# Kernel optimization log

Hardware: AMD Instinct MI355X
Metric: run time of the kernel (lower is better)

Reference implementation:

```python
import jax, jax.numpy as jnp
import numpy as np

N, E, L, D_IN = 20000, 320000, 3, 128
K, H = 8, 64
NEG_SLOPE = 0.01


def setup_inputs() -> dict:
    key = jax.random.key(0)
    k1, k2, k3, k4, k5, k6 = jax.random.split(key, 6)
    return {
        "node_feat": jax.random.normal(k1, (N, D_IN), jnp.float32),
        "edge_feat": jax.random.normal(k2, (E, L, D_IN), jnp.float32),
        "W_enc": jax.random.normal(k3, (D_IN, K * H), jnp.float32) * (1.0 / np.sqrt(D_IN)),
        "attn_l": jax.random.normal(k4, (1, K, H), jnp.float32) * 0.1,
        "W_r": jax.random.normal(k5, (K, D_IN), jnp.float32) * (1.0 / np.sqrt(D_IN)),
        "dst": jax.random.randint(k6, (E,), 0, N, jnp.int32),
    }


def reference(node_feat, edge_feat, W_enc, attn_l, W_r, dst):
    n = node_feat.shape[0]
    e_cnt = edge_feat.shape[0]
    # metapath instance encoder ('linear'): mean over metapath length, then project
    ft = jnp.mean(edge_feat, axis=1) @ W_enc            # (E, K*H)
    ft = ft.reshape(e_cnt, K, H)                        # (E, K, H)
    # per-edge / per-dst attention logits
    el = jnp.sum(ft * attn_l, axis=-1)                  # (E, K)
    er = node_feat @ W_r.T                              # (N, K)
    e = jax.nn.leaky_relu(el + er[dst], negative_slope=NEG_SLOPE)  # (E, K)
    # edge_softmax: segmented (per destination node) stable softmax
    seg_max = jax.ops.segment_max(e, dst, num_segments=n)
    seg_max = jnp.where(jnp.isfinite(seg_max), seg_max, 0.0)
    ex = jnp.exp(e - seg_max[dst])                      # (E, K)
    seg_sum = jax.ops.segment_sum(ex, dst, num_segments=n)
    a = ex / seg_sum[dst]                               # (E, K)  (attn_drop=0 in eval)
    # weighted scatter-sum of edge features into destination nodes
    out = jax.ops.segment_sum(ft * a[..., None], dst, num_segments=n)  # (N, K, H)
    return out
```

## Files before the change

### kernel.cpp

```cpp
#include <hip/hip_runtime.h>
#include <math.h>

#define NN   20000
#define EE   320000
#define DIN  128
#define KK   8
#define HH   64
#define NEG  0.01f
#define CAP  128

typedef __attribute__((ext_vector_type(8))) short short8;
typedef __attribute__((ext_vector_type(4))) float f32x4;

__device__ __forceinline__ unsigned short f2bf(float f) {
  unsigned u = __float_as_uint(f);
  u += 0x7FFF + ((u >> 16) & 1);
  return (unsigned short)(u >> 16);
}
__device__ __forceinline__ float bf2f_lo(unsigned u) {
  return __uint_as_float(u << 16);
}
__device__ __forceinline__ float bf2f_hi(unsigned u) {
  return __uint_as_float(u & 0xFFFF0000u);
}

__device__ __forceinline__ float wave_sum(float v) {
#pragma unroll
  for (int m = 1; m < 64; m <<= 1) v += __shfl_xor(v, m, 64);
  return v;
}

__global__ __launch_bounds__(256) void k_pre(const float* __restrict__ W_enc,
                                             const float* __restrict__ attn_l,
                                             const float* __restrict__ node_feat,
                                             const float* __restrict__ W_r,
                                             unsigned short* __restrict__ Wt,
                                             unsigned short* __restrict__ Vt,
                                             float* __restrict__ er) {
  __shared__ __align__(16) float4 wr4[KK * 32];
  int b = blockIdx.x, tid = threadIdx.x;
  if (b < 256) {
    int gid = b * 256 + tid;
    int row = gid >> 7, d = gid & 127;
    Wt[gid] = f2bf(W_enc[(size_t)d * 512 + row]);
  } else if (b < 264) {
    int gid = (b - 256) * 256 + tid;
    int n = gid >> 7, d = gid & 127;
    float acc = 0.f;
    if (n < 8) {
#pragma unroll 8
      for (int h = 0; h < HH; ++h)
        acc += W_enc[(size_t)d * 512 + n * 64 + h] * attn_l[n * 64 + h];
    }
    Vt[gid] = f2bf(acc);
  } else {
    wr4[tid] = ((const float4*)W_r)[tid];
    __syncthreads();
    int gid = (b - 264) * 256 + tid;
    int n = gid >> 3, k = gid & 7;
    if (n < NN) {
      const float4* nf4 = (const float4*)node_feat + (size_t)n * 32;
      float acc = 0.f;
#pragma unroll
      for (int i = 0; i < 32; ++i) {
        float4 a = nf4[i], bb = wr4[k * 32 + i];
        acc += a.x * bb.x + a.y * bb.y + a.z * bb.z + a.w * bb.w;
      }
      er[gid] = acc;
    }
  }
}

__global__ __launch_bounds__(256) void k_mlog(const float* __restrict__ ef,
                                              const unsigned short* __restrict__ Vt,
                                              const float* __restrict__ er,
                                              const int* __restrict__ dst,
                                              unsigned short* __restrict__ x,
                                              float* __restrict__ e_log,
                                              int* __restrict__ counts) {
  __shared__ __align__(16) uint4 xl4[16 * 17];
  int tid = threadIdx.x;
  size_t gid = (size_t)blockIdx.x * 256 + tid;
  size_t e = gid >> 4;
  int s = gid & 15;
  const float4* p = (const float4*)(ef + e * 384) + s * 2;
  float4 a0 = p[0],  a1 = p[1];
  float4 b0 = p[32], b1 = p[33];
  float4 c0 = p[64], c1 = p[65];
  const float i3 = 1.f / 3.f;
  float m0 = (a0.x + b0.x + c0.x) * i3, m1 = (a0.y + b0.y + c0.y) * i3;
  float m2 = (a0.z + b0.z + c0.z) * i3, m3 = (a0.w + b0.w + c0.w) * i3;
  float m4 = (a1.x + b1.x + c1.x) * i3, m5 = (a1.y + b1.y + c1.y) * i3;
  float m6 = (a1.z + b1.z + c1.z) * i3, m7 = (a1.w + b1.w + c1.w) * i3;
  uint4 o;
  o.x = (unsigned)f2bf(m0) | ((unsigned)f2bf(m1) << 16);
  o.y = (unsigned)f2bf(m2) | ((unsigned)f2bf(m3) << 16);
  o.z = (unsigned)f2bf(m4) | ((unsigned)f2bf(m5) << 16);
  o.w = (unsigned)f2bf(m6) | ((unsigned)f2bf(m7) << 16);
  ((uint4*)x)[gid] = o;
  xl4[(tid >> 4) * 17 + (tid & 15)] = o;
  __syncthreads();

  if (tid < 64) {
    int lane = tid;
    int m = lane & 15, quad = lane >> 4;
    size_t e0 = (size_t)blockIdx.x * 16;
    const short8* xr = (const short8*)((const unsigned short*)xl4 + m * 136);
    const short8* vr = (const short8*)(Vt + (size_t)m * 128);
    f32x4 acc = {0.f, 0.f, 0.f, 0.f};
#pragma unroll
    for (int kt = 0; kt < 4; ++kt) {
      short8 a = xr[kt * 4 + quad];
      short8 bfr = vr[kt * 4 + quad];
      acc = __builtin_amdgcn_mfma_f32_16x16x32_bf16(a, bfr, acc, 0, 0, 0);
    }
    if (m < 8) {
#pragma unroll
      for (int r = 0; r < 4; ++r) {
        size_t ee = e0 + quad * 4 + r;
        int dv = dst[ee];
        float z = acc[r] + er[(size_t)dv * 8 + m];
        z = z > 0.f ? z : NEG * z;
        e_log[ee * 8 + m] = z;
        if (m == 0) atomicAdd(&counts[dv], 1);
      }
    }
  }
}

__device__ __forceinline__ int block_excl_scan256(int v, int tid) {
  __shared__ int wtot[4];
  int lane = tid & 63, wid = tid >> 6;
  int incl = v;
#pragma unroll
  for (int off = 1; off < 64; off <<= 1) {
    int t = __shfl_up(incl, off, 64);
    if (lane >= off) incl += t;
  }
  if (lane == 63) wtot[wid] = incl;
  __syncthreads();
  if (tid == 0) {
    int s = 0;
#pragma unroll
    for (int i = 0; i < 4; ++i) { int t = wtot[i]; wtot[i] = s; s += t; }
  }
  __syncthreads();
  return wtot[wid] + incl - v;
}

__global__ __launch_bounds__(256) void k_scan1(const int* __restrict__ counts,
                                               int* __restrict__ lexcl,
                                               int* __restrict__ btot) {
  int b = blockIdx.x, tid = threadIdx.x;
  int i = b * 256 + tid;
  int v = (i < NN) ? counts[i] : 0;
  int ex = block_excl_scan256(v, tid);
  lexcl[i] = ex;
  if (tid == 255) btot[b] = ex + v;
}

__global__ __launch_bounds__(256) void k_scan2(int* __restrict__ btot,
                                               int* __restrict__ bbase,
                                               int* __restrict__ offs) {
  int tid = threadIdx.x;
  int v = (tid < 80) ? btot[tid] : 0;
  int ex = block_excl_scan256(v, tid);
  if (tid < 80) bbase[tid] = ex;
  if (tid == 0) offs[NN] = EE;
}

__global__ __launch_bounds__(256) void k_scan3(const int* __restrict__ lexcl,
                                               const int* __restrict__ bbase,
                                               int* __restrict__ offs,
                                               int* __restrict__ cursor) {
  int b = blockIdx.x, tid = threadIdx.x;
  int i = b * 256 + tid;
  if (i < NN) {
    int o = lexcl[i] + bbase[b];
    offs[i] = o;
    cursor[i] = o;
  }
}

__global__ __launch_bounds__(256) void k_fill(const int* __restrict__ dst,
                                              int* __restrict__ cursor,
                                              int* __restrict__ elist) {
  int e = blockIdx.x * 256 + threadIdx.x;
  if (e < EE) {
    int p = atomicAdd(&cursor[dst[e]], 1);
    elist[p] = e;
  }
}

__global__ __launch_bounds__(256) void k_agg(const int* __restrict__ offs,
                                             const int* __restrict__ elist,
                                             const float* __restrict__ e_log,
                                             const unsigned short* __restrict__ x,
                                             unsigned short* __restrict__ y) {
  __shared__ float red[4][8];
  __shared__ float maxs[8], invs[8];
  __shared__ int eids[CAP];
  __shared__ __align__(16) float w[CAP * 8];
  __shared__ __align__(16) float xs[32 * 128];
  int n = blockIdx.x;
  int tid = threadIdx.x, lane = tid & 63, wid = tid >> 6;
  int start = offs[n], end = offs[n + 1];
  int cnt = end - start;
  int d = tid & 127, kg = tid >> 7;
  float acc0 = 0.f, acc1 = 0.f, acc2 = 0.f, acc3 = 0.f;

  if (cnt <= CAP) {
    for (int i = tid; i < cnt; i += 256) eids[i] = elist[start + i];
    __syncthreads();
    for (int j = tid; j < cnt * 2; j += 256)
      ((float4*)w)[j] = ((const float4*)e_log)[(size_t)eids[j >> 1] * 2 + (j & 1)];
    __syncthreads();

    int k = tid & 7, ib = tid >> 3;
    float mm = -3.4e38f;
    for (int i = ib; i < cnt; i += 32) mm = fmaxf(mm, w[i * 8 + k]);
    mm = fmaxf(mm, __shfl_xor(mm, 8, 64));
    mm = fmaxf(mm, __shfl_xor(mm, 16, 64));
    mm = fmaxf(mm, __shfl_xor(mm, 32, 64));
    if ((lane >> 3) == 0) red[wid][lane] = mm;
    __syncthreads();
    if (tid < 8)
      maxs[tid] = fmaxf(fmaxf(red[0][tid], red[1][tid]), fmaxf(red[2][tid], red[3][tid]));
    __syncthreads();

    float mk = maxs[k];
    float ss = 0.f;
    for (int i = ib; i < cnt; i += 32) {
      float v = __expf(w[i * 8 + k] - mk);
      w[i * 8 + k] = v;
      ss += v;
    }
    ss += __shfl_xor(ss, 8, 64);
    ss += __shfl_xor(ss, 16, 64);
    ss += __shfl_xor(ss, 32, 64);
    if ((lane >> 3) == 0) red[wid][lane] = ss;
    __syncthreads();
    if (tid < 8) {
      float tot = red[0][tid] + red[1][tid] + red[2][tid] + red[3][tid];
      invs[tid] = tot > 0.f ? 1.f / tot : 0.f;
    }
    __syncthreads();
    float iv = invs[k];
    for (int i = ib; i < cnt; i += 32) w[i * 8 + k] *= iv;
    __syncthreads();

    for (int base = 0; base < cnt; base += 32) {
      int nb = min(32, cnt - base);
      for (int j = tid; j < nb * 16; j += 256) {
        size_t e = (size_t)eids[base + (j >> 4)];
        uint4 t = ((const uint4*)x)[e * 16 + (j & 15)];
        float4 lo = make_float4(bf2f_lo(t.x), bf2f_hi(t.x), bf2f_lo(t.y), bf2f_hi(t.y));
        float4 hi = make_float4(bf2f_lo(t.z), bf2f_hi(t.z), bf2f_lo(t.w), bf2f_hi(t.w));
        ((float4*)xs)[(j >> 4) * 32 + (j & 15) * 2 + 0] = lo;
        ((float4*)xs)[(j >> 4) * 32 + (j & 15) * 2 + 1] = hi;
      }
      __syncthreads();
      for (int j = 0; j < nb; ++j) {
        float xv = xs[j * 128 + d];
        const float* wp = &w[(base + j) * 8 + kg * 4];
        acc0 += wp[0] * xv; acc1 += wp[1] * xv; acc2 += wp[2] * xv; acc3 += wp[3] * xv;
      }
      __syncthreads();
    }
  } else {
    float m8[8];
#pragma unroll
    for (int k = 0; k < 8; ++k) m8[k] = -3.4e38f;
    for (int i = start + tid; i < end; i += 256) {
      size_t e = (size_t)elist[i];
      float4 a = ((const float4*)e_log)[e * 2 + 0];
      float4 b = ((const float4*)e_log)[e * 2 + 1];
      m8[0] = fmaxf(m8[0], a.x); m8[1] = fmaxf(m8[1], a.y);
      m8[2] = fmaxf(m8[2], a.z); m8[3] = fmaxf(m8[3], a.w);
      m8[4] = fmaxf(m8[4], b.x); m8[5] = fmaxf(m8[5], b.y);
      m8[6] = fmaxf(m8[6], b.z); m8[7] = fmaxf(m8[7], b.w);
    }
#pragma unroll
    for (int k = 0; k < 8; ++k) {
#pragma unroll
      for (int mm2 = 1; mm2 < 64; mm2 <<= 1)
        m8[k] = fmaxf(m8[k], __shfl_xor(m8[k], mm2, 64));
    }
    if (lane == 0) {
#pragma unroll
      for (int k = 0; k < 8; ++k) red[wid][k] = m8[k];
    }
    __syncthreads();
    if (tid < 8)
      maxs[tid] = fmaxf(fmaxf(red[0][tid], red[1][tid]), fmaxf(red[2][tid], red[3][tid]));
    __syncthreads();
    float mk8[8];
#pragma unroll
    for (int k = 0; k < 8; ++k) mk8[k] = maxs[k];
    float s8[8];
#pragma unroll
    for (int k = 0; k < 8; ++k) s8[k] = 0.f;
    for (int i = start + tid; i < end; i += 256) {
      size_t e = (size_t)elist[i];
      float4 a = ((const float4*)e_log)[e * 2 + 0];
      float4 b = ((const float4*)e_log)[e * 2 + 1];
      s8[0] += __expf(a.x - mk8[0]); s8[1] += __expf(a.y - mk8[1]);
      s8[2] += __expf(a.z - mk8[2]); s8[3] += __expf(a.w - mk8[3]);
      s8[4] += __expf(b.x - mk8[4]); s8[5] += __expf(b.y - mk8[5]);
      s8[6] += __expf(b.z - mk8[6]); s8[7] += __expf(b.w - mk8[7]);
    }
#pragma unroll
    for (int k = 0; k < 8; ++k) s8[k] = wave_sum(s8[k]);
    if (lane == 0) {
#pragma unroll
      for (int k = 0; k < 8; ++k) red[wid][k] = s8[k];
    }
    __syncthreads();
    if (tid < 8) {
      float tot = red[0][tid] + red[1][tid] + red[2][tid] + red[3][tid];
      invs[tid] = tot > 0.f ? 1.f / tot : 0.f;
    }
    __syncthreads();
    for (int base = start; base < end; base += 32) {
      int nb = min(32, end - base);
      for (int j = tid; j < nb * 16; j += 256) {
        size_t e = (size_t)elist[base + (j >> 4)];
        uint4 t = ((const uint4*)x)[e * 16 + (j & 15)];
        float4 lo = make_float4(bf2f_lo(t.x), bf2f_hi(t.x), bf2f_lo(t.y), bf2f_hi(t.y));
        float4 hi = make_float4(bf2f_lo(t.z), bf2f_hi(t.z), bf2f_lo(t.w), bf2f_hi(t.w));
        ((float4*)xs)[(j >> 4) * 32 + (j & 15) * 2 + 0] = lo;
        ((float4*)xs)[(j >> 4) * 32 + (j & 15) * 2 + 1] = hi;
      }
      if (tid < nb * 8) {
        size_t e = (size_t)elist[base + (tid >> 3)];
        int kk = tid & 7;
        w[tid] = __expf(e_log[e * 8 + kk] - maxs[kk]) * invs[kk];
      }
      __syncthreads();
      for (int j = 0; j < nb; ++j) {
        float xv = xs[j * 128 + d];
        float4 wv = *(const float4*)&w[j * 8 + kg * 4];
        acc0 += wv.x * xv; acc1 += wv.y * xv; acc2 += wv.z * xv; acc3 += wv.w * xv;
      }
      __syncthreads();
    }
  }

  size_t yb = ((size_t)n * 8 + kg * 4) * 128 + d;
  y[yb + 0 * 128] = f2bf(acc0);
  y[yb + 1 * 128] = f2bf(acc1);
  y[yb + 2 * 128] = f2bf(acc2);
  y[yb + 3 * 128] = f2bf(acc3);
}

__global__ __launch_bounds__(256) void k_out(const unsigned short* __restrict__ y,
                                             const unsigned short* __restrict__ Wt,
                                             float* __restrict__ out) {
  int kh = blockIdx.y;
  int n0 = blockIdx.x * 16;
  int wv = threadIdx.x >> 6;
  int lane = threadIdx.x & 63;
  int m = lane & 15, quad = lane >> 4;
  int h0 = wv * 16;
  const short8* ar = (const short8*)(y + ((size_t)(n0 + m) * 8 + kh) * 128);
  const short8* br = (const short8*)(Wt + (size_t)(kh * 64 + h0 + m) * 128);
  f32x4 acc = {0.f, 0.f, 0.f, 0.f};
#pragma unroll
  for (int kt = 0; kt < 4; ++kt) {
    short8 a = ar[kt * 4 + quad];
    short8 b = br[kt * 4 + quad];
    acc = __builtin_amdgcn_mfma_f32_16x16x32_bf16(a, b, acc, 0, 0, 0);
  }
#pragma unroll
  for (int r = 0; r < 4; ++r)
    out[(size_t)(n0 + quad * 4 + r) * 512 + kh * 64 + h0 + m] = acc[r];
}

extern "C" void kernel_launch(void* const* d_in, const int* in_sizes, int n_in,
                              void* d_out, int out_size, void* d_ws, size_t ws_size,
                              hipStream_t stream) {
  const float* node_feat = (const float*)d_in[0];
  const float* edge_feat = (const float*)d_in[1];
  const float* W_enc     = (const float*)d_in[2];
  const float* attn_l    = (const float*)d_in[3];
  const float* W_r       = (const float*)d_in[4];
  const int*   dst       = (const int*)d_in[5];
  float* out = (float*)d_out;

  char* ws = (char*)d_ws;
  size_t off = 0;
  auto carve = [&](size_t bytes) {
    void* p = ws + off;
    off = (off + bytes + 255) & ~(size_t)255;
    return p;
  };
  unsigned short* x   = (unsigned short*)carve((size_t)EE * DIN * 2);
  unsigned short* y   = (unsigned short*)carve((size_t)NN * KK * DIN * 2);
  unsigned short* Vt  = (unsigned short*)carve(16 * 128 * 2);
  unsigned short* Wt  = (unsigned short*)carve((size_t)KK * HH * DIN * 2);
  float* er    = (float*)carve((size_t)NN * KK * 4);
  float* e_log = (float*)carve((size_t)EE * KK * 4);
  int* counts  = (int*)carve((size_t)20480 * 4);
  int* lexcl   = (int*)carve((size_t)20480 * 4);
  int* btot    = (int*)carve(80 * 4);
  int* bbase   = (int*)carve(80 * 4);
  int* offs    = (int*)carve((size_t)(NN + 1) * 4);
  int* cursor  = (int*)carve((size_t)NN * 4);
  int* elist   = (int*)carve((size_t)EE * 4);
  (void)ws_size; (void)in_sizes; (void)n_in; (void)out_size;

  hipMemsetAsync(counts, 0, (size_t)NN * 4, stream);

  k_pre <<<264 + (NN * KK) / 256, 256, 0, stream>>>(W_enc, attn_l, node_feat, W_r,
                                                    Wt, Vt, er);
  k_mlog<<<(EE * 16) / 256, 256, 0, stream>>>(edge_feat, Vt, er, dst, x, e_log, counts);
  k_scan1<<<80, 256, 0, stream>>>(counts, lexcl, btot);
  k_scan2<<<1, 256, 0, stream>>>(btot, bbase, offs);
  k_scan3<<<80, 256, 0, stream>>>(lexcl, bbase, offs, cursor);
  k_fill<<<EE / 256, 256, 0, stream>>>(dst, cursor, elist);
  k_agg <<<NN, 256, 0, stream>>>(offs, elist, e_log, x, y);
  k_out <<<dim3(NN / 16, KK), 256, 0, stream>>>(y, Wt, out);
}
```

Measured before the change: 786.7 us.

## Scatter edge features into dst-sorted order during encoding, drop edge list

Counting of edges per destination moves into the preprocessing kernel, and the prefix scan now runs before the encoder kernel. The encoder claims a slot per edge with an atomic on the cursor and writes its bf16 means and attention logits straight into CSR (dst-sorted) order. This lets the aggregation kernel read contiguous rows instead of gathering through an edge-index list, and it removes the fill kernel and the elist buffer. In exchange the encoder's stores become scattered, and the order of edges within each node depends on atomic ordering, so float sums are not deterministic across runs.

```diff
diff --git a/kernel.cpp b/kernel.cpp
--- a/kernel.cpp
+++ b/kernel.cpp
@@ -34,9 +34,11 @@
                                              const float* __restrict__ attn_l,
                                              const float* __restrict__ node_feat,
                                              const float* __restrict__ W_r,
+                                             const int* __restrict__ dst,
                                              unsigned short* __restrict__ Wt,
                                              unsigned short* __restrict__ Vt,
-                                             float* __restrict__ er) {
+                                             float* __restrict__ er,
+                                             int* __restrict__ counts) {
   __shared__ __align__(16) float4 wr4[KK * 32];
   int b = blockIdx.x, tid = threadIdx.x;
   if (b < 256) {
@@ -53,7 +55,7 @@
         acc += W_enc[(size_t)d * 512 + n * 64 + h] * attn_l[n * 64 + h];
     }
     Vt[gid] = f2bf(acc);
-  } else {
+  } else if (b < 889) {
     wr4[tid] = ((const float4*)W_r)[tid];
     __syncthreads();
     int gid = (b - 264) * 256 + tid;
@@ -68,6 +70,9 @@
       }
       er[gid] = acc;
     }
+  } else {
+    int i = (b - 889) * 256 + tid;
+    atomicAdd(&counts[dst[i]], 1);
   }
 }
 
@@ -75,18 +80,19 @@
                                               const unsigned short* __restrict__ Vt,
                                               const float* __restrict__ er,
                                               const int* __restrict__ dst,
+                                              int* __restrict__ cursor,
                                               unsigned short* __restrict__ x,
-                                              float* __restrict__ e_log,
-                                              int* __restrict__ counts) {
+                                              float* __restrict__ e_log) {
   __shared__ __align__(16) uint4 xl4[16 * 17];
+  __shared__ int pl[16], dl[16];
   int tid = threadIdx.x;
   size_t gid = (size_t)blockIdx.x * 256 + tid;
   size_t e = gid >> 4;
   int s = gid & 15;
-  const float4* p = (const float4*)(ef + e * 384) + s * 2;
-  float4 a0 = p[0],  a1 = p[1];
-  float4 b0 = p[32], b1 = p[33];
-  float4 c0 = p[64], c1 = p[65];
+  const float4* p4 = (const float4*)(ef + e * 384) + s * 2;
+  float4 a0 = p4[0],  a1 = p4[1];
+  float4 b0 = p4[32], b1 = p4[33];
+  float4 c0 = p4[64], c1 = p4[65];
   const float i3 = 1.f / 3.f;
   float m0 = (a0.x + b0.x + c0.x) * i3, m1 = (a0.y + b0.y + c0.y) * i3;
   float m2 = (a0.z + b0.z + c0.z) * i3, m3 = (a0.w + b0.w + c0.w) * i3;
@@ -97,14 +103,21 @@
   o.y = (unsigned)f2bf(m2) | ((unsigned)f2bf(m3) << 16);
   o.z = (unsigned)f2bf(m4) | ((unsigned)f2bf(m5) << 16);
   o.w = (unsigned)f2bf(m6) | ((unsigned)f2bf(m7) << 16);
-  ((uint4*)x)[gid] = o;
-  xl4[(tid >> 4) * 17 + (tid & 15)] = o;
+  xl4[(tid >> 4) * 17 + s] = o;
+
+  if (tid < 16) {
+    int ee = blockIdx.x * 16 + tid;
+    int dv = dst[ee];
+    pl[tid] = atomicAdd(&cursor[dv], 1);
+    dl[tid] = dv;
+  }
   __syncthreads();
+
+  ((uint4*)x)[(size_t)pl[tid >> 4] * 16 + s] = o;
 
   if (tid < 64) {
     int lane = tid;
     int m = lane & 15, quad = lane >> 4;
-    size_t e0 = (size_t)blockIdx.x * 16;
     const short8* xr = (const short8*)((const unsigned short*)xl4 + m * 136);
     const short8* vr = (const short8*)(Vt + (size_t)m * 128);
     f32x4 acc = {0.f, 0.f, 0.f, 0.f};
@@ -117,12 +130,11 @@
     if (m < 8) {
 #pragma unroll
       for (int r = 0; r < 4; ++r) {
-        size_t ee = e0 + quad * 4 + r;
-        int dv = dst[ee];
+        int le = quad * 4 + r;
+        int dv = dl[le];
         float z = acc[r] + er[(size_t)dv * 8 + m];
         z = z > 0.f ? z : NEG * z;
-        e_log[ee * 8 + m] = z;
-        if (m == 0) atomicAdd(&counts[dv], 1);
+        e_log[(size_t)pl[le] * 8 + m] = z;
       }
     }
   }
@@ -182,24 +194,12 @@
   }
 }
 
-__global__ __launch_bounds__(256) void k_fill(const int* __restrict__ dst,
-                                              int* __restrict__ cursor,
-                                              int* __restrict__ elist) {
-  int e = blockIdx.x * 256 + threadIdx.x;
-  if (e < EE) {
-    int p = atomicAdd(&cursor[dst[e]], 1);
-    elist[p] = e;
-  }
-}
-
 __global__ __launch_bounds__(256) void k_agg(const int* __restrict__ offs,
-                                             const int* __restrict__ elist,
                                              const float* __restrict__ e_log,
                                              const unsigned short* __restrict__ x,
                                              unsigned short* __restrict__ y) {
   __shared__ float red[4][8];
   __shared__ float maxs[8], invs[8];
-  __shared__ int eids[CAP];
   __shared__ __align__(16) float w[CAP * 8];
   __shared__ __align__(16) float xs[32 * 128];
   int n = blockIdx.x;
@@ -210,10 +210,8 @@
   float acc0 = 0.f, acc1 = 0.f, acc2 = 0.f, acc3 = 0.f;
 
   if (cnt <= CAP) {
-    for (int i = tid; i < cnt; i += 256) eids[i] = elist[start + i];
-    __syncthreads();
     for (int j = tid; j < cnt * 2; j += 256)
-      ((float4*)w)[j] = ((const float4*)e_log)[(size_t)eids[j >> 1] * 2 + (j & 1)];
+      ((float4*)w)[j] = ((const float4*)e_log)[(size_t)start * 2 + j];
     __syncthreads();
 
     int k = tid & 7, ib = tid >> 3;
@@ -252,8 +250,7 @@
     for (int base = 0; base < cnt; base += 32) {
       int nb = min(32, cnt - base);
       for (int j = tid; j < nb * 16; j += 256) {
-        size_t e = (size_t)eids[base + (j >> 4)];
-        uint4 t = ((const uint4*)x)[e * 16 + (j & 15)];
+        uint4 t = ((const uint4*)x)[((size_t)start + base) * 16 + j];
         float4 lo = make_float4(bf2f_lo(t.x), bf2f_hi(t.x), bf2f_lo(t.y), bf2f_hi(t.y));
         float4 hi = make_float4(bf2f_lo(t.z), bf2f_hi(t.z), bf2f_lo(t.w), bf2f_hi(t.w));
         ((float4*)xs)[(j >> 4) * 32 + (j & 15) * 2 + 0] = lo;
@@ -271,10 +268,9 @@
     float m8[8];
 #pragma unroll
     for (int k = 0; k < 8; ++k) m8[k] = -3.4e38f;
-    for (int i = start + tid; i < end; i += 256) {
-      size_t e = (size_t)elist[i];
-      float4 a = ((const float4*)e_log)[e * 2 + 0];
-      float4 b = ((const float4*)e_log)[e * 2 + 1];
+    for (int i = tid; i < cnt; i += 256) {
+      float4 a = ((const float4*)e_log)[((size_t)start + i) * 2 + 0];
+      float4 b = ((const float4*)e_log)[((size_t)start + i) * 2 + 1];
       m8[0] = fmaxf(m8[0], a.x); m8[1] = fmaxf(m8[1], a.y);
       m8[2] = fmaxf(m8[2], a.z); m8[3] = fmaxf(m8[3], a.w);
       m8[4] = fmaxf(m8[4], b.x); m8[5] = fmaxf(m8[5], b.y);
@@ -300,10 +296,9 @@
     float s8[8];
 #pragma unroll
     for (int k = 0; k < 8; ++k) s8[k] = 0.f;
-    for (int i = start + tid; i < end; i += 256) {
-      size_t e = (size_t)elist[i];
-      float4 a = ((const float4*)e_log)[e * 2 + 0];
-      float4 b = ((const float4*)e_log)[e * 2 + 1];
+    for (int i = tid; i < cnt; i += 256) {
+      float4 a = ((const float4*)e_log)[((size_t)start + i) * 2 + 0];
+      float4 b = ((const float4*)e_log)[((size_t)start + i) * 2 + 1];
       s8[0] += __expf(a.x - mk8[0]); s8[1] += __expf(a.y - mk8[1]);
       s8[2] += __expf(a.z - mk8[2]); s8[3] += __expf(a.w - mk8[3]);
       s8[4] += __expf(b.x - mk8[4]); s8[5] += __expf(b.y - mk8[5]);
@@ -321,20 +316,18 @@
       invs[tid] = tot > 0.f ? 1.f / tot : 0.f;
     }
     __syncthreads();
-    for (int base = start; base < end; base += 32) {
-      int nb = min(32, end - base);
+    for (int base = 0; base < cnt; base += 32) {
+      int nb = min(32, cnt - base);
       for (int j = tid; j < nb * 16; j += 256) {
-        size_t e = (size_t)elist[base + (j >> 4)];
-        uint4 t = ((const uint4*)x)[e * 16 + (j & 15)];
+        uint4 t = ((const uint4*)x)[((size_t)start + base) * 16 + j];
         float4 lo = make_float4(bf2f_lo(t.x), bf2f_hi(t.x), bf2f_lo(t.y), bf2f_hi(t.y));
         float4 hi = make_float4(bf2f_lo(t.z), bf2f_hi(t.z), bf2f_lo(t.w), bf2f_hi(t.w));
         ((float4*)xs)[(j >> 4) * 32 + (j & 15) * 2 + 0] = lo;
         ((float4*)xs)[(j >> 4) * 32 + (j & 15) * 2 + 1] = hi;
       }
       if (tid < nb * 8) {
-        size_t e = (size_t)elist[base + (tid >> 3)];
         int kk = tid & 7;
-        w[tid] = __expf(e_log[e * 8 + kk] - maxs[kk]) * invs[kk];
+        w[tid] = __expf(e_log[((size_t)start + base + (tid >> 3)) * 8 + kk] - maxs[kk]) * invs[kk];
       }
       __syncthreads();
       for (int j = 0; j < nb; ++j) {
@@ -406,18 +399,16 @@
   int* bbase   = (int*)carve(80 * 4);
   int* offs    = (int*)carve((size_t)(NN + 1) * 4);
   int* cursor  = (int*)carve((size_t)NN * 4);
-  int* elist   = (int*)carve((size_t)EE * 4);
   (void)ws_size; (void)in_sizes; (void)n_in; (void)out_size;
 
   hipMemsetAsync(counts, 0, (size_t)NN * 4, stream);
 
-  k_pre <<<264 + (NN * KK) / 256, 256, 0, stream>>>(W_enc, attn_l, node_feat, W_r,
-                                                    Wt, Vt, er);
-  k_mlog<<<(EE * 16) / 256, 256, 0, stream>>>(edge_feat, Vt, er, dst, x, e_log, counts);
+  k_pre <<<889 + EE / 256, 256, 0, stream>>>(W_enc, attn_l, node_feat, W_r, dst,
+                                             Wt, Vt, er, counts);
   k_scan1<<<80, 256, 0, stream>>>(counts, lexcl, btot);
   k_scan2<<<1, 256, 0, stream>>>(btot, bbase, offs);
   k_scan3<<<80, 256, 0, stream>>>(lexcl, bbase, offs, cursor);
-  k_fill<<<EE / 256, 256, 0, stream>>>(dst, cursor, elist);
-  k_agg <<<NN, 256, 0, stream>>>(offs, elist, e_log, x, y);
+  k_mlog<<<(EE * 16) / 256, 256, 0, stream>>>(edge_feat, Vt, er, dst, cursor, x, e_log);
+  k_agg <<<NN, 256, 0, stream>>>(offs, e_log, x, y);
   k_out <<<dim3(NN / 16, KK), 256, 0, stream>>>(y, Wt, out);
 }
```

Result: no change. 779.5 us (-0.9%).
